# Performance work log

Measured on AMD Instinct MI355X. Metric: run time of the kernel, lower is better.

## Reference

```python
import jax, jax.numpy as jnp
import numpy as np

B, L, C, H = 256, 256, 512, 512
MOG_ITERS = 5

def _xavier(key, shape):
    fan_in, fan_out = shape[0], shape[1]
    lim = jnp.sqrt(6.0 / (fan_in + fan_out))
    return jax.random.uniform(key, shape, jnp.float32, -lim, lim)

def setup_inputs() -> dict:
    key = jax.random.key(0)
    ks = jax.random.split(key, 7)
    x = jax.random.normal(ks[0], (B, L, C), jnp.float32)
    # Linear weights stored as (in, out); torch Linear computes x @ W.T + b, identical math.
    Wih_w = _xavier(ks[1], (C, 4 * H)); Wih_b = jnp.zeros((4 * H,), jnp.float32)
    Wmx_w = _xavier(ks[2], (C, H));     Wmx_b = jnp.zeros((H,), jnp.float32)
    Wmh_w = _xavier(ks[3], (H, H));     Wmh_b = jnp.zeros((H,), jnp.float32)
    Whm_w = _xavier(ks[4], (H, 4 * H)); Whm_b = jnp.zeros((4 * H,), jnp.float32)
    Q = _xavier(ks[5], (H, C))  # ht @ Q -> (B, C)
    R = _xavier(ks[6], (C, H))  # xt @ R -> (B, H)
    return {"x": x, "Wih_w": Wih_w, "Wih_b": Wih_b, "Wmx_w": Wmx_w, "Wmx_b": Wmx_b,
            "Wmh_w": Wmh_w, "Wmh_b": Wmh_b, "Whm_w": Whm_w, "Whm_b": Whm_b, "Q": Q, "R": R}

def reference(x, Wih_w, Wih_b, Wmx_w, Wmx_b, Wmh_w, Wmh_b, Whm_w, Whm_b, Q, R):
    batch = x.shape[0]
    h0 = jnp.zeros((batch, H), x.dtype)
    c0 = jnp.zeros((batch, H), x.dtype)

    def step(carry, xt):
        ht, Ct = carry
        # Mogrify: odd iters update xt, even iters update ht
        for i in range(1, MOG_ITERS + 1):
            if i % 2 == 0:
                ht = 2.0 * jax.nn.sigmoid(xt @ R) * ht
            else:
                xt = 2.0 * jax.nn.sigmoid(ht @ Q) * xt
        mt = (xt @ Wmx_w + Wmx_b) + (ht @ Wmh_w + Wmh_b)
        gates = (xt @ Wih_w + Wih_b) + (mt @ Whm_w + Whm_b)
        ingate, forgetgate, cellgate, outgate = jnp.split(gates, 4, axis=1)
        ft = jax.nn.sigmoid(forgetgate)
        it = jax.nn.sigmoid(ingate)
        cand = jnp.tanh(cellgate)
        ot = jax.nn.sigmoid(outgate)
        Ct = ft * Ct + it * cand
        ht = ot * jnp.tanh(Ct)
        return (ht, Ct), ht

    xs = jnp.swapaxes(x, 0, 1)  # (L, B, C)
    _, hs = jax.lax.scan(step, (h0, c0), xs)
    return jnp.swapaxes(hs, 0, 1)  # (B, L, H)
```

## Files before the change

### kernel.cpp

```cpp
#include <hip/hip_runtime.h>
#include <hip/hip_bf16.h>
#include <cmath>

typedef __attribute__((ext_vector_type(8))) short short8;
typedef __attribute__((ext_vector_type(4))) float f32x4;
typedef __attribute__((ext_vector_type(2))) float f32x2;
typedef __attribute__((ext_vector_type(4))) unsigned int u32x4;

union AFu { u32x4 v; short8 s; };

__device__ inline float bf2f(ushort u) {
    unsigned v = (unsigned)u << 16; float f; __builtin_memcpy(&f, &v, 4); return f;
}
__device__ inline ushort f2bf(float f) {
    __hip_bfloat16 h = __float2bfloat16(f); ushort u; __builtin_memcpy(&u, &h, 2); return u;
}
__device__ inline float sigf(float z) { return 1.f / (1.f + expf(-z)); }

__device__ __forceinline__ void sysst32(void* p, unsigned v) {
    __hip_atomic_store((unsigned*)p, v, __ATOMIC_RELAXED, __HIP_MEMORY_SCOPE_SYSTEM);
}

#define BB 256
#define LL 256
#define HH 512
#define G4 2048

__device__ __forceinline__ unsigned swz(unsigned row, unsigned byteInRow) {
    return (row * 1024u + byteInRow) ^ ((row & 7u) << 4);
}

__device__ __forceinline__ void stage_A16(const ushort* Ag, int r0, ushort* Ast, int tid) {
    const char* src = (const char*)(Ag + (size_t)(r0 + (tid >> 4)) * HH + (tid & 15) * 32);
    u32x4 v0, v1, v2, v3;
    asm volatile(
        "global_load_dwordx4 %0, %4, off sc0 sc1\n\t"
        "global_load_dwordx4 %1, %4, off offset:16 sc0 sc1\n\t"
        "global_load_dwordx4 %2, %4, off offset:32 sc0 sc1\n\t"
        "global_load_dwordx4 %3, %4, off offset:48 sc0 sc1\n\t"
        "s_waitcnt vmcnt(0)"
        : "=&v"(v0), "=&v"(v1), "=&v"(v2), "=&v"(v3) : "v"(src) : "memory");
    unsigned row = (unsigned)(tid >> 4), b = (unsigned)((tid & 15) * 64);
    *(u32x4*)((char*)Ast + swz(row, b))      = v0;
    *(u32x4*)((char*)Ast + swz(row, b + 16)) = v1;
    *(u32x4*)((char*)Ast + swz(row, b + 32)) = v2;
    *(u32x4*)((char*)Ast + swz(row, b + 48)) = v3;
}

__device__ __forceinline__ void rb_arrive(unsigned* slots, int sub, unsigned epoch) {
    asm volatile("s_waitcnt vmcnt(0)" ::: "memory");
    __syncthreads();
    if (threadIdx.x == 0)
        __hip_atomic_store(slots + sub, epoch, __ATOMIC_RELAXED, __HIP_MEMORY_SCOPE_AGENT);
}
__device__ __forceinline__ void rb_wait(unsigned* slots, unsigned epoch) {
    if (threadIdx.x < 16)
        while (__hip_atomic_load(slots + threadIdx.x, __ATOMIC_RELAXED,
                                 __HIP_MEMORY_SCOPE_AGENT) < epoch)
            __builtin_amdgcn_s_sleep(1);
    __syncthreads();
}


__global__ __launch_bounds__(256) void init_state(ushort* hp) {
    int i = blockIdx.x * 256 + threadIdx.x;
    hp[i] = 0;
}

__global__ __launch_bounds__(256) void transpose_f32_bf16(
    const float* __restrict__ in, ushort* __restrict__ out, int K, int N)
{
    __shared__ float tile[32][33];
    int tx = threadIdx.x & 31, ty = threadIdx.x >> 5;
    int bk = blockIdx.x * 32, bn = blockIdx.y * 32;
    #pragma unroll
    for (int i = 0; i < 32; i += 8)
        tile[ty + i][tx] = in[(size_t)(bk + ty + i) * N + (bn + tx)];
    __syncthreads();
    #pragma unroll
    for (int i = 0; i < 32; i += 8)
        out[(size_t)(bn + ty + i) * K + (bk + tx)] = f2bf(tile[tx][ty + i]);
}

__global__ __launch_bounds__(256) void combine_w(
    const float* __restrict__ base, const float* __restrict__ A,
    const float* __restrict__ Bm, float* __restrict__ out, int use_base)
{
    int n  = blockIdx.x * 256 + threadIdx.x;
    int k0 = blockIdx.y * 8;
    float acc[8];
    #pragma unroll
    for (int r = 0; r < 8; ++r)
        acc[r] = use_base ? base[(size_t)(k0 + r) * G4 + n] : 0.f;
    for (int m = 0; m < 512; ++m) {
        float bv = Bm[(size_t)m * G4 + n];
        #pragma unroll
        for (int r = 0; r < 8; ++r)
            acc[r] = fmaf(A[(size_t)(k0 + r) * 512 + m], bv, acc[r]);
    }
    #pragma unroll
    for (int r = 0; r < 8; ++r) out[(size_t)(k0 + r) * G4 + n] = acc[r];
}

__global__ __launch_bounds__(256) void bias_g_kernel(
    const float* __restrict__ Wih_b, const float* __restrict__ Whm_b,
    const float* __restrict__ Wmx_b, const float* __restrict__ Wmh_b,
    const float* __restrict__ Whm, float* __restrict__ bias_g)
{
    int n = blockIdx.x * 256 + threadIdx.x;
    float acc = Wih_b[n] + Whm_b[n];
    for (int m = 0; m < 512; ++m)
        acc = fmaf(Wmx_b[m] + Wmh_b[m], Whm[(size_t)m * G4 + n], acc);
    bias_g[n] = acc;
}


__device__ __forceinline__ void mog_stage_p(
    const ushort* Ast,
    const ushort* Wlds,
    ushort (*myBuf)[32], ushort* __restrict__ outG,
    const float* __restrict__ xscale, float (*pbuf)[16][16],
    int r0, int cs, int t, int tid)
{
    int lane = tid & 63, wave = tid >> 6;
    int lr = lane & 15, lk = lane >> 4;
    int ct = wave & 1, kh = wave >> 1;
    int colloc = ct * 16 + lr;

    float xs[4];
    if (xscale != nullptr && kh == 0) {
        #pragma unroll
        for (int r = 0; r < 4; ++r)
            xs[r] = xscale[((size_t)(r0 + lk * 4 + r) * LL + t) * HH + cs * 32 + colloc];
    }

    f32x4 acc = {0.f, 0.f, 0.f, 0.f};
    #pragma unroll
    for (int kk = 0; kk < 8; ++kk) {
        short8 a = *(const short8*)((const char*)Ast +
                     swz((unsigned)lr, (unsigned)(kh * 512 + kk * 64 + lk * 16)));
        short8 b = *(const short8*)((const char*)Wlds +
                     swz((unsigned)colloc, (unsigned)(kh * 512 + kk * 64 + lk * 16)));
        acc = __builtin_amdgcn_mfma_f32_16x16x32_bf16(a, b, acc, 0, 0, 0);
    }

    if (kh == 1) {
        #pragma unroll
        for (int r = 0; r < 4; ++r) pbuf[ct][lk * 4 + r][lr] = acc[r];
    }
    __syncthreads();
    if (kh == 0) {
        #pragma unroll
        for (int r = 0; r < 4; ++r) {
            float v = acc[r] + pbuf[ct][lk * 4 + r][lr];
            float sc = (xscale != nullptr) ? xs[r] : bf2f(myBuf[lk * 4 + r][colloc]);
            myBuf[lk * 4 + r][colloc] = f2bf(2.f * sigf(v) * sc);
        }
    }
    __syncthreads();
    {
        int row = tid >> 4, c2 = tid & 15;
        unsigned v = *(const unsigned*)&myBuf[row][c2 * 2];
        sysst32((char*)outG + (((size_t)(r0 + row)) * HH + cs * 32 + c2 * 2) * 2, v);
    }
}

__global__ __launch_bounds__(256) void moglstm_persistent(
    const float* __restrict__ x,
    const ushort* __restrict__ QT, const ushort* __restrict__ RT,
    const ushort* __restrict__ W1T, const ushort* __restrict__ W2T,
    const float* __restrict__ biasg,
    ushort* __restrict__ hp, ushort* __restrict__ xa, ushort* __restrict__ hb1,
    ushort* __restrict__ xb, ushort* __restrict__ hb2, ushort* __restrict__ xc,
    float* __restrict__ out, unsigned* __restrict__ flags)
{
    __shared__ ushort QTs[32 * 512];
    __shared__ ushort RTs[32 * 512];
    __shared__ ushort Ast[16 * 512];
    __shared__ float  pbuf[2][16][16];
    __shared__ ushort myX[16][32];
    __shared__ ushort myH[16][32];
    __shared__ float  gbuf[4][16][32];

    int tid = threadIdx.x;
    int rb = blockIdx.x >> 4, cs = blockIdx.x & 15;
    int r0 = rb * 16;
    int lane = tid & 63, wave = tid >> 6;
    int lr = lane & 15, lk = lane >> 4;

    #pragma unroll
    for (int i = 0; i < 8; ++i) {
        int ch = i * 256 + tid, col = ch >> 6, kc = ch & 63;
        *(u32x4*)((char*)QTs + swz((unsigned)col, (unsigned)(kc * 16))) =
            *(const u32x4*)(QT + (size_t)(cs * 32 + col) * HH + kc * 8);
        *(u32x4*)((char*)RTs + swz((unsigned)col, (unsigned)(kc * 16))) =
            *(const u32x4*)(RT + (size_t)(cs * 32 + col) * HH + kc * 8);
    }
    ((unsigned*)myH)[tid] = 0;
    float Creg0 = 0.f, Creg1 = 0.f;
    __syncthreads();

    unsigned* slots = flags + rb * 16;

    for (int t = 0; t < LL; ++t) {
        unsigned ep = (unsigned)t * 6u;

        stage_A16(hp, r0, Ast, tid); __syncthreads();
        mog_stage_p(Ast, QTs, myX, xa, x, pbuf, r0, cs, t, tid);
        rb_arrive(slots, cs, ep + 1); rb_wait(slots, ep + 1);
        stage_A16(xa, r0, Ast, tid); __syncthreads();
        mog_stage_p(Ast, RTs, myH, hb1, nullptr, pbuf, r0, cs, t, tid);
        rb_arrive(slots, cs, ep + 2); rb_wait(slots, ep + 2);
        stage_A16(hb1, r0, Ast, tid); __syncthreads();
        mog_stage_p(Ast, QTs, myX, xb, nullptr, pbuf, r0, cs, t, tid);
        rb_arrive(slots, cs, ep + 3); rb_wait(slots, ep + 3);
        stage_A16(xb, r0, Ast, tid); __syncthreads();
        mog_stage_p(Ast, RTs, myH, hb2, nullptr, pbuf, r0, cs, t, tid);
        rb_arrive(slots, cs, ep + 4); rb_wait(slots, ep + 4);

        stage_A16(hb2, r0, Ast, tid); __syncthreads();
        mog_stage_p(Ast, QTs, myX, xc, nullptr, pbuf, r0, cs, t, tid);
        rb_arrive(slots, cs, ep + 5);

        int q = wave;
        f32x4 acc0 = {0,0,0,0}, acc1 = {0,0,0,0};
        {
            const short8* B0 = (const short8*)(W2T + (size_t)(q * 512 + cs * 32 + lr) * HH);
            const short8* B1 = (const short8*)(W2T + (size_t)(q * 512 + cs * 32 + 16 + lr) * HH);
            #pragma unroll
            for (int kk = 0; kk < 16; ++kk) {
                short8 a = *(const short8*)((const char*)Ast +
                             swz((unsigned)lr, (unsigned)(kk * 64 + lk * 16)));
                acc0 = __builtin_amdgcn_mfma_f32_16x16x32_bf16(a, B0[kk * 4 + lk], acc0, 0, 0, 0);
                acc1 = __builtin_amdgcn_mfma_f32_16x16x32_bf16(a, B1[kk * 4 + lk], acc1, 0, 0, 0);
            }
        }
        rb_wait(slots, ep + 5);

        stage_A16(xc, r0, Ast, tid); __syncthreads();
        {
            const short8* B0 = (const short8*)(W1T + (size_t)(q * 512 + cs * 32 + lr) * HH);
            const short8* B1 = (const short8*)(W1T + (size_t)(q * 512 + cs * 32 + 16 + lr) * HH);
            #pragma unroll
            for (int kk = 0; kk < 16; ++kk) {
                short8 a = *(const short8*)((const char*)Ast +
                             swz((unsigned)lr, (unsigned)(kk * 64 + lk * 16)));
                acc0 = __builtin_amdgcn_mfma_f32_16x16x32_bf16(a, B0[kk * 4 + lk], acc0, 0, 0, 0);
                acc1 = __builtin_amdgcn_mfma_f32_16x16x32_bf16(a, B1[kk * 4 + lk], acc1, 0, 0, 0);
            }
        }
        {
            float b0 = biasg[q * 512 + cs * 32 + lr];
            float b1 = biasg[q * 512 + cs * 32 + 16 + lr];
            #pragma unroll
            for (int r = 0; r < 4; ++r) {
                gbuf[q][lk * 4 + r][lr]      = acc0[r] + b0;
                gbuf[q][lk * 4 + r][16 + lr] = acc1[r] + b1;
            }
        }
        __syncthreads();
        {
            int row = tid >> 4, c2 = tid & 15;
            int colg = cs * 32 + c2 * 2;
            float i0 = sigf(gbuf[0][row][c2 * 2]),      f0 = sigf(gbuf[1][row][c2 * 2]);
            float g0 = tanhf(gbuf[2][row][c2 * 2]),     o0 = sigf(gbuf[3][row][c2 * 2]);
            Creg0 = f0 * Creg0 + i0 * g0;
            float h0v = o0 * tanhf(Creg0);
            float i1 = sigf(gbuf[0][row][c2 * 2 + 1]),  f1 = sigf(gbuf[1][row][c2 * 2 + 1]);
            float g1 = tanhf(gbuf[2][row][c2 * 2 + 1]), o1 = sigf(gbuf[3][row][c2 * 2 + 1]);
            Creg1 = f1 * Creg1 + i1 * g1;
            float h1v = o1 * tanhf(Creg1);
            f32x2 hv2 = {h0v, h1v};
            *(f32x2*)(out + ((size_t)(r0 + row) * LL + t) * HH + colg) = hv2;
            unsigned hu = (unsigned)f2bf(h0v) | ((unsigned)f2bf(h1v) << 16);
            sysst32((char*)hp + (((size_t)(r0 + row)) * HH + colg) * 2, hu);
            *(unsigned*)&myH[row][c2 * 2] = hu;
        }
        rb_arrive(slots, cs, ep + 6); rb_wait(slots, ep + 6);
    }
}

extern "C" void kernel_launch(void* const* d_in, const int* in_sizes, int n_in,
                              void* d_out, int out_size, void* d_ws, size_t ws_size,
                              hipStream_t stream)
{
    const float* x     = (const float*)d_in[0];
    const float* Wih_w = (const float*)d_in[1];
    const float* Wih_b = (const float*)d_in[2];
    const float* Wmx_w = (const float*)d_in[3];
    const float* Wmx_b = (const float*)d_in[4];
    const float* Wmh_w = (const float*)d_in[5];
    const float* Wmh_b = (const float*)d_in[6];
    const float* Whm_w = (const float*)d_in[7];
    const float* Whm_b = (const float*)d_in[8];
    const float* Q     = (const float*)d_in[9];
    const float* R     = (const float*)d_in[10];
    float* out = (float*)d_out;

    char* ws = (char*)d_ws;
    ushort* QT   = (ushort*)ws;               ws += (size_t)512 * 512 * 2;
    ushort* RT   = (ushort*)ws;               ws += (size_t)512 * 512 * 2;
    ushort* W1T  = (ushort*)ws;               ws += (size_t)G4  * 512 * 2;
    ushort* W2T  = (ushort*)ws;               ws += (size_t)G4  * 512 * 2;
    float*  biasg= (float*)ws;                ws += (size_t)G4 * 4;
    ushort* xa   = (ushort*)ws;               ws += (size_t)BB * HH * 2;
    ushort* hb1  = (ushort*)ws;               ws += (size_t)BB * HH * 2;
    ushort* xb   = (ushort*)ws;               ws += (size_t)BB * HH * 2;
    ushort* hb2  = (ushort*)ws;               ws += (size_t)BB * HH * 2;
    ushort* xc   = (ushort*)ws;               ws += (size_t)BB * HH * 2;
    ushort* hp   = (ushort*)ws;               ws += (size_t)BB * HH * 2;
    float*  Wtmp = (float*)ws;                ws += (size_t)512 * G4 * 4;

    unsigned* flags = (unsigned*)Wtmp;

    init_state<<<512, 256, 0, stream>>>(hp);
    transpose_f32_bf16<<<dim3(16, 16), 256, 0, stream>>>(Q, QT, 512, 512);
    transpose_f32_bf16<<<dim3(16, 16), 256, 0, stream>>>(R, RT, 512, 512);
    combine_w<<<dim3(8, 64), 256, 0, stream>>>(Wih_w, Wmx_w, Whm_w, Wtmp, 1);
    transpose_f32_bf16<<<dim3(16, 64), 256, 0, stream>>>(Wtmp, W1T, 512, G4);
    combine_w<<<dim3(8, 64), 256, 0, stream>>>(nullptr, Wmh_w, Whm_w, Wtmp, 0);
    transpose_f32_bf16<<<dim3(16, 64), 256, 0, stream>>>(Wtmp, W2T, 512, G4);
    bias_g_kernel<<<8, 256, 0, stream>>>(Wih_b, Whm_b, Wmx_b, Wmh_b, Whm_w, biasg);
    hipMemsetAsync(flags, 0, (size_t)16 * 16 * sizeof(unsigned), stream);

    moglstm_persistent<<<256, 256, 0, stream>>>(x, QT, RT, W1T, W2T, biasg,
                                                hp, xa, hb1, xb, hb2, xc, out, flags);
}
```

Measured before the change: 7.270 ms.

## Load activation fragments directly into registers and reuse across gate GEMMs

```diff
diff --git a/kernel.cpp b/kernel.cpp
--- a/kernel.cpp
+++ b/kernel.cpp
@@ -4,7 +4,6 @@
 
 typedef __attribute__((ext_vector_type(8))) short short8;
 typedef __attribute__((ext_vector_type(4))) float f32x4;
-typedef __attribute__((ext_vector_type(2))) float f32x2;
 typedef __attribute__((ext_vector_type(4))) unsigned int u32x4;
 
 union AFu { u32x4 v; short8 s; };
@@ -19,6 +18,26 @@
 
 __device__ __forceinline__ void sysst32(void* p, unsigned v) {
     __hip_atomic_store((unsigned*)p, v, __ATOMIC_RELAXED, __HIP_MEMORY_SCOPE_SYSTEM);
+}
+
+__device__ __forceinline__ void ld8_s128(const void* base,
+    u32x4& a0, u32x4& a1, u32x4& a2, u32x4& a3,
+    u32x4& a4, u32x4& a5, u32x4& a6, u32x4& a7)
+{
+    asm volatile(
+        "global_load_dwordx4 %0, %8, off sc0 sc1\n\t"
+        "global_load_dwordx4 %1, %8, off offset:128 sc0 sc1\n\t"
+        "global_load_dwordx4 %2, %8, off offset:256 sc0 sc1\n\t"
+        "global_load_dwordx4 %3, %8, off offset:384 sc0 sc1\n\t"
+        "global_load_dwordx4 %4, %8, off offset:512 sc0 sc1\n\t"
+        "global_load_dwordx4 %5, %8, off offset:640 sc0 sc1\n\t"
+        "global_load_dwordx4 %6, %8, off offset:768 sc0 sc1\n\t"
+        "global_load_dwordx4 %7, %8, off offset:896 sc0 sc1\n\t"
+        "s_waitcnt vmcnt(0)"
+        : "=&v"(a0), "=&v"(a1), "=&v"(a2), "=&v"(a3),
+          "=&v"(a4), "=&v"(a5), "=&v"(a6), "=&v"(a7)
+        : "v"(base)
+        : "memory");
 }
 
 #define BB 256
@@ -28,23 +47,6 @@
 
 __device__ __forceinline__ unsigned swz(unsigned row, unsigned byteInRow) {
     return (row * 1024u + byteInRow) ^ ((row & 7u) << 4);
-}
-
-__device__ __forceinline__ void stage_A16(const ushort* Ag, int r0, ushort* Ast, int tid) {
-    const char* src = (const char*)(Ag + (size_t)(r0 + (tid >> 4)) * HH + (tid & 15) * 32);
-    u32x4 v0, v1, v2, v3;
-    asm volatile(
-        "global_load_dwordx4 %0, %4, off sc0 sc1\n\t"
-        "global_load_dwordx4 %1, %4, off offset:16 sc0 sc1\n\t"
-        "global_load_dwordx4 %2, %4, off offset:32 sc0 sc1\n\t"
-        "global_load_dwordx4 %3, %4, off offset:48 sc0 sc1\n\t"
-        "s_waitcnt vmcnt(0)"
-        : "=&v"(v0), "=&v"(v1), "=&v"(v2), "=&v"(v3) : "v"(src) : "memory");
-    unsigned row = (unsigned)(tid >> 4), b = (unsigned)((tid & 15) * 64);
-    *(u32x4*)((char*)Ast + swz(row, b))      = v0;
-    *(u32x4*)((char*)Ast + swz(row, b + 16)) = v1;
-    *(u32x4*)((char*)Ast + swz(row, b + 32)) = v2;
-    *(u32x4*)((char*)Ast + swz(row, b + 48)) = v3;
 }
 
 __device__ __forceinline__ void rb_arrive(unsigned* slots, int sub, unsigned epoch) {
@@ -115,41 +117,44 @@
 }
 
 
-__device__ __forceinline__ void mog_stage_p(
-    const ushort* Ast,
-    const ushort* Wlds,
+__device__ __forceinline__ void mog2(
+    const ushort* __restrict__ Ag, const ushort* Wlds,
     ushort (*myBuf)[32], ushort* __restrict__ outG,
     const float* __restrict__ xscale, float (*pbuf)[16][16],
-    int r0, int cs, int t, int tid)
+    int r0, int cs, int t, int tid,
+    u32x4& a0, u32x4& a1, u32x4& a2, u32x4& a3,
+    u32x4& a4, u32x4& a5, u32x4& a6, u32x4& a7)
 {
     int lane = tid & 63, wave = tid >> 6;
     int lr = lane & 15, lk = lane >> 4;
-    int ct = wave & 1, kh = wave >> 1;
+    int kp = wave >> 1, ct = wave & 1;
     int colloc = ct * 16 + lr;
 
     float xs[4];
-    if (xscale != nullptr && kh == 0) {
+    if (xscale != nullptr && kp == 0) {
         #pragma unroll
         for (int r = 0; r < 4; ++r)
             xs[r] = xscale[((size_t)(r0 + lk * 4 + r) * LL + t) * HH + cs * 32 + colloc];
     }
 
+    const char* Ab = (const char*)(Ag + (size_t)(r0 + lr) * HH) + kp * 64 + lk * 16;
+    ld8_s128(Ab, a0, a1, a2, a3, a4, a5, a6, a7);
+
     f32x4 acc = {0.f, 0.f, 0.f, 0.f};
-    #pragma unroll
-    for (int kk = 0; kk < 8; ++kk) {
-        short8 a = *(const short8*)((const char*)Ast +
-                     swz((unsigned)lr, (unsigned)(kh * 512 + kk * 64 + lk * 16)));
-        short8 b = *(const short8*)((const char*)Wlds +
-                     swz((unsigned)colloc, (unsigned)(kh * 512 + kk * 64 + lk * 16)));
-        acc = __builtin_amdgcn_mfma_f32_16x16x32_bf16(a, b, acc, 0, 0, 0);
-    }
-
-    if (kh == 1) {
+#define MOGMF(i, ai) { AFu u; u.v = ai;                                          \
+        short8 b = *(const short8*)((const char*)Wlds +                          \
+            swz((unsigned)colloc, (unsigned)((2 * i + kp) * 64 + lk * 16)));     \
+        acc = __builtin_amdgcn_mfma_f32_16x16x32_bf16(u.s, b, acc, 0, 0, 0); }
+    MOGMF(0, a0) MOGMF(1, a1) MOGMF(2, a2) MOGMF(3, a3)
+    MOGMF(4, a4) MOGMF(5, a5) MOGMF(6, a6) MOGMF(7, a7)
+#undef MOGMF
+
+    if (kp == 1) {
         #pragma unroll
         for (int r = 0; r < 4; ++r) pbuf[ct][lk * 4 + r][lr] = acc[r];
     }
     __syncthreads();
-    if (kh == 0) {
+    if (kp == 0) {
         #pragma unroll
         for (int r = 0; r < 4; ++r) {
             float v = acc[r] + pbuf[ct][lk * 4 + r][lr];
@@ -176,17 +181,21 @@
 {
     __shared__ ushort QTs[32 * 512];
     __shared__ ushort RTs[32 * 512];
-    __shared__ ushort Ast[16 * 512];
     __shared__ float  pbuf[2][16][16];
     __shared__ ushort myX[16][32];
     __shared__ ushort myH[16][32];
     __shared__ float  gbuf[4][16][32];
+    __shared__ ushort padl[4096];
 
     int tid = threadIdx.x;
+    asm volatile("" :: "v"((unsigned)(size_t)&padl[0]));
+
     int rb = blockIdx.x >> 4, cs = blockIdx.x & 15;
     int r0 = rb * 16;
     int lane = tid & 63, wave = tid >> 6;
     int lr = lane & 15, lk = lane >> 4;
+    int kp = wave >> 1, ct = wave & 1;
+    int colloc = ct * 16 + lr;
 
     #pragma unroll
     for (int i = 0; i < 8; ++i) {
@@ -197,84 +206,78 @@
             *(const u32x4*)(RT + (size_t)(cs * 32 + col) * HH + kc * 8);
     }
     ((unsigned*)myH)[tid] = 0;
-    float Creg0 = 0.f, Creg1 = 0.f;
+    float Creg[4] = {0.f, 0.f, 0.f, 0.f};
     __syncthreads();
 
     unsigned* slots = flags + rb * 16;
+    u32x4 a0, a1, a2, a3, a4, a5, a6, a7;
 
     for (int t = 0; t < LL; ++t) {
         unsigned ep = (unsigned)t * 6u;
-
-        stage_A16(hp, r0, Ast, tid); __syncthreads();
-        mog_stage_p(Ast, QTs, myX, xa, x, pbuf, r0, cs, t, tid);
+        mog2(hp, QTs, myX, xa, x, pbuf, r0, cs, t, tid, a0, a1, a2, a3, a4, a5, a6, a7);
         rb_arrive(slots, cs, ep + 1); rb_wait(slots, ep + 1);
-        stage_A16(xa, r0, Ast, tid); __syncthreads();
-        mog_stage_p(Ast, RTs, myH, hb1, nullptr, pbuf, r0, cs, t, tid);
+        mog2(xa, RTs, myH, hb1, nullptr, pbuf, r0, cs, t, tid, a0, a1, a2, a3, a4, a5, a6, a7);
         rb_arrive(slots, cs, ep + 2); rb_wait(slots, ep + 2);
-        stage_A16(hb1, r0, Ast, tid); __syncthreads();
-        mog_stage_p(Ast, QTs, myX, xb, nullptr, pbuf, r0, cs, t, tid);
+        mog2(hb1, QTs, myX, xb, nullptr, pbuf, r0, cs, t, tid, a0, a1, a2, a3, a4, a5, a6, a7);
         rb_arrive(slots, cs, ep + 3); rb_wait(slots, ep + 3);
-        stage_A16(xb, r0, Ast, tid); __syncthreads();
-        mog_stage_p(Ast, RTs, myH, hb2, nullptr, pbuf, r0, cs, t, tid);
+        mog2(xb, RTs, myH, hb2, nullptr, pbuf, r0, cs, t, tid, a0, a1, a2, a3, a4, a5, a6, a7);
         rb_arrive(slots, cs, ep + 4); rb_wait(slots, ep + 4);
-
-        stage_A16(hb2, r0, Ast, tid); __syncthreads();
-        mog_stage_p(Ast, QTs, myX, xc, nullptr, pbuf, r0, cs, t, tid);
+        mog2(hb2, QTs, myX, xc, nullptr, pbuf, r0, cs, t, tid, a0, a1, a2, a3, a4, a5, a6, a7);
         rb_arrive(slots, cs, ep + 5);
 
-        int q = wave;
-        f32x4 acc0 = {0,0,0,0}, acc1 = {0,0,0,0};
-        {
-            const short8* B0 = (const short8*)(W2T + (size_t)(q * 512 + cs * 32 + lr) * HH);
-            const short8* B1 = (const short8*)(W2T + (size_t)(q * 512 + cs * 32 + 16 + lr) * HH);
+        f32x4 g0 = {0,0,0,0}, g1 = {0,0,0,0}, g2 = {0,0,0,0}, g3 = {0,0,0,0};
+#define GQ(gq, q, Wt) {                                                           \
+        const short8* Bq = (const short8*)(Wt + (size_t)(q * 512 + cs * 32 + colloc) * HH); \
+        AFu u;                                                                    \
+        u.v = a0; gq = __builtin_amdgcn_mfma_f32_16x16x32_bf16(u.s, Bq[(0*2+kp)*4+lk], gq, 0,0,0); \
+        u.v = a1; gq = __builtin_amdgcn_mfma_f32_16x16x32_bf16(u.s, Bq[(1*2+kp)*4+lk], gq, 0,0,0); \
+        u.v = a2; gq = __builtin_amdgcn_mfma_f32_16x16x32_bf16(u.s, Bq[(2*2+kp)*4+lk], gq, 0,0,0); \
+        u.v = a3; gq = __builtin_amdgcn_mfma_f32_16x16x32_bf16(u.s, Bq[(3*2+kp)*4+lk], gq, 0,0,0); \
+        u.v = a4; gq = __builtin_amdgcn_mfma_f32_16x16x32_bf16(u.s, Bq[(4*2+kp)*4+lk], gq, 0,0,0); \
+        u.v = a5; gq = __builtin_amdgcn_mfma_f32_16x16x32_bf16(u.s, Bq[(5*2+kp)*4+lk], gq, 0,0,0); \
+        u.v = a6; gq = __builtin_amdgcn_mfma_f32_16x16x32_bf16(u.s, Bq[(6*2+kp)*4+lk], gq, 0,0,0); \
+        u.v = a7; gq = __builtin_amdgcn_mfma_f32_16x16x32_bf16(u.s, Bq[(7*2+kp)*4+lk], gq, 0,0,0); }
+        GQ(g0, 0, W2T) GQ(g1, 1, W2T) GQ(g2, 2, W2T) GQ(g3, 3, W2T)
+        rb_wait(slots, ep + 5);
+
+        ld8_s128((const char*)(xc + (size_t)(r0 + lr) * HH) + kp * 64 + lk * 16,
+                 a0, a1, a2, a3, a4, a5, a6, a7);
+        GQ(g0, 0, W1T) GQ(g1, 1, W1T) GQ(g2, 2, W1T) GQ(g3, 3, W1T)
+#undef GQ
+
+        if (kp == 1) {
             #pragma unroll
-            for (int kk = 0; kk < 16; ++kk) {
-                short8 a = *(const short8*)((const char*)Ast +
-                             swz((unsigned)lr, (unsigned)(kk * 64 + lk * 16)));
-                acc0 = __builtin_amdgcn_mfma_f32_16x16x32_bf16(a, B0[kk * 4 + lk], acc0, 0, 0, 0);
-                acc1 = __builtin_amdgcn_mfma_f32_16x16x32_bf16(a, B1[kk * 4 + lk], acc1, 0, 0, 0);
+            for (int r = 0; r < 4; ++r) {
+                gbuf[0][lk * 4 + r][colloc] = g0[r];
+                gbuf[1][lk * 4 + r][colloc] = g1[r];
+                gbuf[2][lk * 4 + r][colloc] = g2[r];
+                gbuf[3][lk * 4 + r][colloc] = g3[r];
             }
         }
-        rb_wait(slots, ep + 5);
-
-        stage_A16(xc, r0, Ast, tid); __syncthreads();
-        {
-            const short8* B0 = (const short8*)(W1T + (size_t)(q * 512 + cs * 32 + lr) * HH);
-            const short8* B1 = (const short8*)(W1T + (size_t)(q * 512 + cs * 32 + 16 + lr) * HH);
-            #pragma unroll
-            for (int kk = 0; kk < 16; ++kk) {
-                short8 a = *(const short8*)((const char*)Ast +
-                             swz((unsigned)lr, (unsigned)(kk * 64 + lk * 16)));
-                acc0 = __builtin_amdgcn_mfma_f32_16x16x32_bf16(a, B0[kk * 4 + lk], acc0, 0, 0, 0);
-                acc1 = __builtin_amdgcn_mfma_f32_16x16x32_bf16(a, B1[kk * 4 + lk], acc1, 0, 0, 0);
-            }
-        }
-        {
-            float b0 = biasg[q * 512 + cs * 32 + lr];
-            float b1 = biasg[q * 512 + cs * 32 + 16 + lr];
+        __syncthreads();
+        if (kp == 0) {
+            float b0 = biasg[0 * 512 + cs * 32 + colloc];
+            float b1 = biasg[1 * 512 + cs * 32 + colloc];
+            float b2 = biasg[2 * 512 + cs * 32 + colloc];
+            float b3 = biasg[3 * 512 + cs * 32 + colloc];
             #pragma unroll
             for (int r = 0; r < 4; ++r) {
-                gbuf[q][lk * 4 + r][lr]      = acc0[r] + b0;
-                gbuf[q][lk * 4 + r][16 + lr] = acc1[r] + b1;
+                int row = lk * 4 + r;
+                float gi = sigf(g0[r] + gbuf[0][row][colloc] + b0);
+                float gf = sigf(g1[r] + gbuf[1][row][colloc] + b1);
+                float gc = tanhf(g2[r] + gbuf[2][row][colloc] + b2);
+                float go = sigf(g3[r] + gbuf[3][row][colloc] + b3);
+                Creg[r] = gf * Creg[r] + gi * gc;
+                float h = go * tanhf(Creg[r]);
+                out[((size_t)(r0 + row) * LL + t) * HH + cs * 32 + colloc] = h;
+                myH[row][colloc] = f2bf(h);
             }
         }
         __syncthreads();
         {
             int row = tid >> 4, c2 = tid & 15;
-            int colg = cs * 32 + c2 * 2;
-            float i0 = sigf(gbuf[0][row][c2 * 2]),      f0 = sigf(gbuf[1][row][c2 * 2]);
-            float g0 = tanhf(gbuf[2][row][c2 * 2]),     o0 = sigf(gbuf[3][row][c2 * 2]);
-            Creg0 = f0 * Creg0 + i0 * g0;
-            float h0v = o0 * tanhf(Creg0);
-            float i1 = sigf(gbuf[0][row][c2 * 2 + 1]),  f1 = sigf(gbuf[1][row][c2 * 2 + 1]);
-            float g1 = tanhf(gbuf[2][row][c2 * 2 + 1]), o1 = sigf(gbuf[3][row][c2 * 2 + 1]);
-            Creg1 = f1 * Creg1 + i1 * g1;
-            float h1v = o1 * tanhf(Creg1);
-            f32x2 hv2 = {h0v, h1v};
-            *(f32x2*)(out + ((size_t)(r0 + row) * LL + t) * HH + colg) = hv2;
-            unsigned hu = (unsigned)f2bf(h0v) | ((unsigned)f2bf(h1v) << 16);
-            sysst32((char*)hp + (((size_t)(r0 + row)) * HH + colg) * 2, hu);
-            *(unsigned*)&myH[row][c2 * 2] = hu;
+            unsigned v = *(const unsigned*)&myH[row][c2 * 2];
+            sysst32((char*)hp + (((size_t)(r0 + row)) * HH + cs * 32 + c2 * 2) * 2, v);
         }
         rb_arrive(slots, cs, ep + 6); rb_wait(slots, ep + 6);
     }
```

After: 7.851 ms. +8.0%, slower.
